# Kernel tuning notes

Hardware: AMD Instinct MI355X
Metric: run time of the kernel (lower is better)

Reference implementation:

```python
import jax, jax.numpy as jnp
import numpy as np


def setup_inputs() -> dict:
    key = jax.random.key(0)
    k1, _ = jax.random.split(key)
    B, H, W, C = 8, 128, 128, 512
    inputs = jax.random.normal(k1, (B, H, W, C), dtype=jnp.float32)
    gamma = jnp.ones((), dtype=jnp.float32)
    return {"inputs": inputs, "gamma": gamma}


def reference(inputs, gamma):
    B, H, W, C = inputs.shape
    q = inputs.reshape(B, H * W, C).astype(jnp.float32)  # [B, HW, C]
    # attention = key @ query = q^T q  -> [B, C, C]
    attn = jnp.einsum('bnc,bnd->bcd', q, q)
    # reversed-softmax trick: softmax(max - attn) over last axis
    attn = jnp.max(attn, axis=-1, keepdims=True) - attn
    attn = jax.nn.softmax(attn, axis=-1)
    # value = query @ attention -> [B, HW, C]
    value = jnp.einsum('bnc,bcd->bnd', q, attn)
    value = value.astype(inputs.dtype).reshape(B, H, W, C)
    return gamma * value + inputs
```

## Files before the change

kernel.cpp:

```cpp
#include <hip/hip_runtime.h>
#include <hip/hip_bf16.h>

#define B_  8
#define C_  512
#define NN  16384
#define SPL 8
#define KB_ (NN / SPL)
#define TT  (KB_ / 64)

typedef _Float16 half8 __attribute__((ext_vector_type(8)));
typedef float    f32x4 __attribute__((ext_vector_type(4)));

__device__ __forceinline__ unsigned short f2h(float x) {
    union { _Float16 h; unsigned short u; } cv;
    cv.h = (_Float16)x;
    return cv.u;
}

__device__ __forceinline__ void gload16(const unsigned short* src, unsigned short* ldst) {
    __builtin_amdgcn_global_load_lds(
        (const __attribute__((address_space(1))) void*)src,
        (__attribute__((address_space(3))) void*)ldst,
        16, 0, 0);
}

__global__ void ws_probe_kernel(float* out, float v) { out[0] = v; }

__global__ __launch_bounds__(256) void pack_kernel(const float* __restrict__ in,
                                                   unsigned short* __restrict__ qT) {
    __shared__ unsigned short lh[64][72];
    int t  = threadIdx.x;
    int n0 = blockIdx.x * 64;
    int c0 = blockIdx.y * 64;
    int b  = blockIdx.z;
    const float* ib = in + ((size_t)b * NN + n0) * C_ + c0;
#pragma unroll
    for (int p = 0; p < 4; ++p) {
        int nl = p * 16 + (t >> 4);
        int cl = (t & 15) * 4;
        float4 v = *(const float4*)(ib + (size_t)nl * C_ + cl);
        lh[cl + 0][nl] = f2h(v.x);
        lh[cl + 1][nl] = f2h(v.y);
        lh[cl + 2][nl] = f2h(v.z);
        lh[cl + 3][nl] = f2h(v.w);
    }
    __syncthreads();
    size_t obase = ((size_t)b * C_ + c0) * NN + n0;
#pragma unroll
    for (int p = 0; p < 2; ++p) {
        int cr = p * 32 + (t >> 3);
        int nf = (t & 7) * 8;
        *(uint4*)(qT + obase + (size_t)cr * NN + nf) = *(const uint4*)&lh[cr][nf];
    }
}

__global__ __launch_bounds__(512, 2) void gram_kernel(const unsigned short* __restrict__ qT,
                                                      float* __restrict__ P) {
    __shared__ unsigned short sA[2][16384];
    __shared__ unsigned short sB[2][16384];
    int t = threadIdx.x, lane = t & 63, wave = t >> 6;
    int wr = wave >> 2, wc = wave & 3;
    int bid = blockIdx.x;
    int b = bid & 7, r = bid >> 3;
    int tile = r & 3, split = r >> 2;
    int tc = tile >> 1, td = tile & 1;
    size_t qb = (size_t)b * C_ * NN;
    const unsigned short* Ap = qT + qb + (size_t)(tc * 256) * NN + (size_t)split * KB_;
    const unsigned short* Bp = qT + qb + (size_t)(td * 256) * NN + (size_t)split * KB_;

    f32x4 acc[8][4];
#pragma unroll
    for (int m = 0; m < 8; ++m)
#pragma unroll
        for (int n = 0; n < 4; ++n) acc[m][n] = (f32x4){0.f, 0.f, 0.f, 0.f};

    int o0 = t * 16,         u0 = o0 ^ (((o0 >> 9) & 1) << 5);
    int o1 = (t + 512) * 16, u1 = o1 ^ (((o1 >> 9) & 1) << 5);
    int rih0 = u0 >> 7, k0 = (u0 & 127) >> 1;
    int rih1 = u1 >> 7, k1 = (u1 & 127) >> 1;

#define STAGE(dst, dd, h, panel, kt)                                                        \
    do {                                                                                    \
        gload16((panel) + (size_t)((h)*128 + rih0) * NN + (kt)*64 + k0,                     \
                &dst[dd][(h)*8192 + t * 8]);                                                \
        gload16((panel) + (size_t)((h)*128 + rih1) * NN + (kt)*64 + k1,                     \
                &dst[dd][(h)*8192 + (t + 512) * 8]);                                        \
    } while (0)

    int g16 = (lane >> 4) * 16;
#define AFRAG(dd, row, ks) \
    (*(const half8*)((const char*)&sA[dd][0] + (((row)*128 + (ks)*64 + g16) ^ (((row)&4) << 3))))
#define BFRAG(dd, row, ks) \
    (*(const half8*)((const char*)&sB[dd][0] + (((row)*128 + (ks)*64 + g16) ^ (((row)&4) << 3))))

    STAGE(sA, 0, 0, Ap, 0);
    STAGE(sB, 0, 0, Bp, 0);
    STAGE(sB, 0, 1, Bp, 0);
    STAGE(sA, 0, 1, Ap, 0);
    asm volatile("s_waitcnt vmcnt(2)" ::: "memory");
    __builtin_amdgcn_s_barrier();

    for (int kt = 0; kt < TT; ++kt) {
        int d = kt & 1, nd = d ^ 1;
        half8 aF[4][2], b0F[2][2], b1F[2][2];
#pragma unroll
        for (int m = 0; m < 4; ++m) {
            int row = wr * 64 + m * 16 + (lane & 15);
#pragma unroll
            for (int ks = 0; ks < 2; ++ks) aF[m][ks] = AFRAG(d, row, ks);
        }
#pragma unroll
        for (int n = 0; n < 2; ++n) {
            int row0 = wc * 32 + n * 16 + (lane & 15);
#pragma unroll
            for (int ks = 0; ks < 2; ++ks) {
                b0F[n][ks] = BFRAG(d, row0, ks);
                b1F[n][ks] = BFRAG(d, (row0 + 128), ks);
            }
        }
        if (kt + 1 < TT) {
            STAGE(sA, nd, 0, Ap, kt + 1);
            STAGE(sB, nd, 0, Bp, kt + 1);
            STAGE(sB, nd, 1, Bp, kt + 1);
        }
        __builtin_amdgcn_s_setprio(1);
#pragma unroll
        for (int m = 0; m < 4; ++m)
#pragma unroll
            for (int n = 0; n < 2; ++n)
#pragma unroll
                for (int ks = 0; ks < 2; ++ks) {
                    acc[m][n]     = __builtin_amdgcn_mfma_f32_16x16x32_f16(aF[m][ks], b0F[n][ks], acc[m][n],     0, 0, 0);
                    acc[m][n + 2] = __builtin_amdgcn_mfma_f32_16x16x32_f16(aF[m][ks], b1F[n][ks], acc[m][n + 2], 0, 0, 0);
                }
        __builtin_amdgcn_s_setprio(0);
        if (kt + 1 < TT) {
            asm volatile("s_waitcnt vmcnt(6)" ::: "memory");
        } else {
            asm volatile("s_waitcnt vmcnt(0)" ::: "memory");
        }
        __builtin_amdgcn_s_barrier();
#pragma unroll
        for (int m = 0; m < 4; ++m) {
            int row = 128 + wr * 64 + m * 16 + (lane & 15);
#pragma unroll
            for (int ks = 0; ks < 2; ++ks) aF[m][ks] = AFRAG(d, row, ks);
        }
        if (kt + 1 < TT) STAGE(sA, nd, 1, Ap, kt + 1);
        __builtin_amdgcn_s_setprio(1);
#pragma unroll
        for (int m = 0; m < 4; ++m)
#pragma unroll
            for (int n = 0; n < 2; ++n)
#pragma unroll
                for (int ks = 0; ks < 2; ++ks) {
                    acc[m + 4][n + 2] = __builtin_amdgcn_mfma_f32_16x16x32_f16(aF[m][ks], b1F[n][ks], acc[m + 4][n + 2], 0, 0, 0);
                    acc[m + 4][n]     = __builtin_amdgcn_mfma_f32_16x16x32_f16(aF[m][ks], b0F[n][ks], acc[m + 4][n],     0, 0, 0);
                }
        __builtin_amdgcn_s_setprio(0);
        asm volatile("s_waitcnt vmcnt(2)" ::: "memory");
        __builtin_amdgcn_s_barrier();
    }

    float* out = P + ((size_t)(split * 8 + b)) * (C_ * C_);
#pragma unroll
    for (int m = 0; m < 8; ++m) {
        int row0 = tc * 256 + wr * 64 + (m & 3) * 16 + (m >> 2) * 128 + (lane >> 4) * 4;
#pragma unroll
        for (int n = 0; n < 4; ++n) {
            int col = td * 256 + wc * 32 + (n & 1) * 16 + (n >> 1) * 128 + (lane & 15);
#pragma unroll
            for (int j = 0; j < 4; ++j)
                out[(size_t)(row0 + j) * C_ + col] = acc[m][n][j];
        }
    }
#undef STAGE
#undef AFRAG
#undef BFRAG
}

__global__ __launch_bounds__(256) void softmax_kernel(const float* __restrict__ P,
                                                      unsigned short* __restrict__ WT) {
    __shared__ unsigned short lw[C_ * 4];
    int t = threadIdx.x, lane = t & 63, wave = t >> 6;
    int b = blockIdx.y;
    int c = blockIdx.x * 4 + wave;
    const float* base = P + (size_t)b * (C_ * C_) + (size_t)c * C_;

    float g[8];
    float mn = 3.4e38f;
#pragma unroll
    for (int k = 0; k < 8; ++k) {
        int d = k * 64 + lane;
        float v = 0.f;
#pragma unroll
        for (int s = 0; s < 8; ++s) v += base[(size_t)s * (8 * C_ * C_) + d];
        g[k] = v;
        mn = fminf(mn, v);
    }
#pragma unroll
    for (int o = 32; o; o >>= 1) mn = fminf(mn, __shfl_xor(mn, o));
    float w[8];
    float sum = 0.f;
#pragma unroll
    for (int k = 0; k < 8; ++k) { w[k] = __expf(mn - g[k]); sum += w[k]; }
#pragma unroll
    for (int o = 32; o; o >>= 1) sum += __shfl_xor(sum, o);
    float inv = 1.0f / sum;
#pragma unroll
    for (int k = 0; k < 8; ++k) {
        int d = k * 64 + lane;
        lw[d * 4 + wave] = f2h(w[k] * inv);
    }
    __syncthreads();
    int c0 = blockIdx.x * 4;
    for (int d = t; d < C_; d += 256)
        *(ushort4*)(WT + ((size_t)b * C_ + d) * C_ + c0) = *(ushort4*)&lw[d * 4];
}

__global__ __launch_bounds__(512, 4) void value_kernel(const float* __restrict__ in,
                                                       const unsigned short* __restrict__ WT,
                                                       const float* __restrict__ gamma,
                                                       float* __restrict__ out) {
    __shared__ unsigned short vA[2][64 * 32];
    __shared__ unsigned short vB[2][512 * 32];
    int t = threadIdx.x, lane = t & 63, wave = t >> 6;
    int wr = wave >> 2, wc = wave & 3;
    int bid = blockIdx.x;
    int b = bid & 7, nt = bid >> 3;
    const float* Ain = in + ((size_t)b * NN + (size_t)nt * 64) * C_;
    const unsigned short* Bin = WT + (size_t)b * C_ * C_;

    f32x4 acc[2][8];
#pragma unroll
    for (int m = 0; m < 2; ++m)
#pragma unroll
        for (int n = 0; n < 8; ++n) acc[m][n] = (f32x4){0.f, 0.f, 0.f, 0.f};

    int boff[4];
#pragma unroll
    for (int p = 0; p < 4; ++p) {
        int o = (t + p * 512) * 16;
        int u = o ^ (((o >> 7) & 3) << 4);
        boff[p] = (u >> 6) * C_ + ((u & 63) >> 1);
    }
    int arow = t >> 2, apart = t & 3;
    bool doA = (t < 256);
    int aoff = arow * C_ + apart * 8;
    int awr  = (arow * 64 + apart * 16) ^ ((arow & 7) << 4);

    auto stageB = [&](int nb, int kt) {
#pragma unroll
        for (int p = 0; p < 4; ++p)
            gload16(Bin + (size_t)boff[p] + kt * 32, &vB[nb][(t + p * 512) * 8]);
    };
    auto loadA = [&](int kt, float4* rg) {
        if (doA) {
            const float* s = Ain + aoff + kt * 32;
            rg[0] = *(const float4*)(s + 0);
            rg[1] = *(const float4*)(s + 4);
        }
    };
    auto writeA = [&](int nb, const float4* rg) {
        if (doA) {
            const float* f = (const float*)rg;
            half8 h;
#pragma unroll
            for (int j = 0; j < 8; ++j) h[j] = (_Float16)f[j];
            *(half8*)((char*)&vA[nb][0] + awr) = h;
        }
    };

    float4 a0[2];
    loadA(0, a0);
    stageB(0, 0);
    writeA(0, a0);
    __syncthreads();

    int g16 = (lane >> 4) * 16;
    for (int kt = 0; kt < 16; ++kt) {
        int cur = kt & 1;
        const char* pa = (const char*)&vA[cur][0];
        const char* pb = (const char*)&vB[cur][0];
        half8 aF[2], bF0[4], bF1[4];
#pragma unroll
        for (int m = 0; m < 2; ++m) {
            int row = wr * 32 + m * 16 + (lane & 15);
            aF[m] = *(const half8*)(pa + ((row * 64 + g16) ^ ((row & 7) << 4)));
        }
#pragma unroll
        for (int n = 0; n < 4; ++n) {
            int row = wc * 128 + n * 16 + (lane & 15);
            bF0[n] = *(const half8*)(pb + ((row * 64 + g16) ^ (((row >> 1) & 3) << 4)));
        }
        float4 an[2];
        if (kt < 15) { loadA(kt + 1, an); stageB(cur ^ 1, kt + 1); }
        __builtin_amdgcn_s_setprio(1);
#pragma unroll
        for (int m = 0; m < 2; ++m)
#pragma unroll
            for (int n = 0; n < 4; ++n)
                acc[m][n] = __builtin_amdgcn_mfma_f32_16x16x32_f16(aF[m], bF0[n], acc[m][n], 0, 0, 0);
        __builtin_amdgcn_s_setprio(0);
#pragma unroll
        for (int n = 0; n < 4; ++n) {
            int row = wc * 128 + (n + 4) * 16 + (lane & 15);
            bF1[n] = *(const half8*)(pb + ((row * 64 + g16) ^ (((row >> 1) & 3) << 4)));
        }
        __builtin_amdgcn_s_setprio(1);
#pragma unroll
        for (int m = 0; m < 2; ++m)
#pragma unroll
            for (int n = 0; n < 4; ++n)
                acc[m][n + 4] = __builtin_amdgcn_mfma_f32_16x16x32_f16(aF[m], bF1[n], acc[m][n + 4], 0, 0, 0);
        __builtin_amdgcn_s_setprio(0);
        if (kt < 15) writeA(cur ^ 1, an);
        __syncthreads();
    }

    float gm = gamma[0];
#pragma unroll
    for (int m = 0; m < 2; ++m) {
        int nrow0 = nt * 64 + wr * 32 + m * 16 + (lane >> 4) * 4;
#pragma unroll
        for (int n = 0; n < 8; ++n) {
            int dd = wc * 128 + n * 16 + (lane & 15);
#pragma unroll
            for (int j = 0; j < 4; ++j) {
                size_t idx = ((size_t)b * NN + (nrow0 + j)) * C_ + dd;
                out[idx] = gm * acc[m][n][j] + in[idx];
            }
        }
    }
}

extern "C" void kernel_launch(void* const* d_in, const int* in_sizes, int n_in,
                              void* d_out, int out_size, void* d_ws, size_t ws_size,
                              hipStream_t stream) {
    const float* in    = (const float*)d_in[0];
    const float* gamma = (const float*)d_in[1];
    float* out = (float*)d_out;

    const size_t q_elems = (size_t)B_ * C_ * NN;
    const size_t need = q_elems * 2
                      + (size_t)SPL * B_ * C_ * C_ * 4
                      + (size_t)B_ * C_ * C_ * 2;
    if (ws_size < need) {
        ws_probe_kernel<<<1, 1, 0, stream>>>(out, (float)ws_size);
        return;
    }

    unsigned short* qT = (unsigned short*)d_ws;
    float* P = (float*)(qT + q_elems);
    unsigned short* WT = (unsigned short*)(P + (size_t)SPL * B_ * C_ * C_);

    pack_kernel<<<dim3(NN / 64, C_ / 64, B_), 256, 0, stream>>>(in, qT);
    gram_kernel<<<256, 512, 0, stream>>>(qT, P);
    softmax_kernel<<<dim3(C_ / 4, B_), 256, 0, stream>>>(P, WT);
    value_kernel<<<2048, 512, 0, stream>>>(in, WT, gamma, out);
}
```

Measured before the change: 350.1 us.

## Stage full fp16 A tile in LDS, read B directly, reuse tile for residual

The value kernel now converts the block's whole 64x512 input tile to fp16 in LDS once, instead of double-buffering 32-wide K slices. B fragments are loaded straight from global memory per lane rather than staged through LDS. This removes the per-iteration barriers from the main loop. The epilogue takes the residual from the fp16 LDS copy instead of re-reading the fp32 input, which saves global traffic but rounds the residual term to fp16. The 64KB of LDS per block may lower occupancy, and the uncoalesced B loads now depend on the cache.

```diff
diff --git a/kernel.cpp b/kernel.cpp
--- a/kernel.cpp
+++ b/kernel.cpp
@@ -222,8 +222,7 @@
                                                        const unsigned short* __restrict__ WT,
                                                        const float* __restrict__ gamma,
                                                        float* __restrict__ out) {
-    __shared__ unsigned short vA[2][64 * 32];
-    __shared__ unsigned short vB[2][512 * 32];
+    __shared__ unsigned short vA[64 * 512];
     int t = threadIdx.x, lane = t & 63, wave = t >> 6;
     int wr = wave >> 2, wc = wave & 3;
     int bid = blockIdx.x;
@@ -231,104 +230,66 @@
     const float* Ain = in + ((size_t)b * NN + (size_t)nt * 64) * C_;
     const unsigned short* Bin = WT + (size_t)b * C_ * C_;
 
+#pragma unroll
+    for (int i = 0; i < 8; ++i) {
+        int chunk = i * 512 + t;
+        int rr = chunk >> 6, c8 = (chunk & 63) * 8;
+        const float* s = Ain + (size_t)rr * C_ + c8;
+        float4 v0 = *(const float4*)s;
+        float4 v1 = *(const float4*)(s + 4);
+        half8 h;
+        h[0] = (_Float16)v0.x; h[1] = (_Float16)v0.y; h[2] = (_Float16)v0.z; h[3] = (_Float16)v0.w;
+        h[4] = (_Float16)v1.x; h[5] = (_Float16)v1.y; h[6] = (_Float16)v1.z; h[7] = (_Float16)v1.w;
+        *(half8*)((char*)vA + ((rr * 1024 + c8 * 2) ^ ((rr & 7) << 4))) = h;
+    }
+    __syncthreads();
+
     f32x4 acc[2][8];
 #pragma unroll
     for (int m = 0; m < 2; ++m)
 #pragma unroll
         for (int n = 0; n < 8; ++n) acc[m][n] = (f32x4){0.f, 0.f, 0.f, 0.f};
 
-    int boff[4];
-#pragma unroll
-    for (int p = 0; p < 4; ++p) {
-        int o = (t + p * 512) * 16;
-        int u = o ^ (((o >> 7) & 3) << 4);
-        boff[p] = (u >> 6) * C_ + ((u & 63) >> 1);
-    }
-    int arow = t >> 2, apart = t & 3;
-    bool doA = (t < 256);
-    int aoff = arow * C_ + apart * 8;
-    int awr  = (arow * 64 + apart * 16) ^ ((arow & 7) << 4);
-
-    auto stageB = [&](int nb, int kt) {
-#pragma unroll
-        for (int p = 0; p < 4; ++p)
-            gload16(Bin + (size_t)boff[p] + kt * 32, &vB[nb][(t + p * 512) * 8]);
-    };
-    auto loadA = [&](int kt, float4* rg) {
-        if (doA) {
-            const float* s = Ain + aoff + kt * 32;
-            rg[0] = *(const float4*)(s + 0);
-            rg[1] = *(const float4*)(s + 4);
-        }
-    };
-    auto writeA = [&](int nb, const float4* rg) {
-        if (doA) {
-            const float* f = (const float*)rg;
-            half8 h;
-#pragma unroll
-            for (int j = 0; j < 8; ++j) h[j] = (_Float16)f[j];
-            *(half8*)((char*)&vA[nb][0] + awr) = h;
-        }
-    };
-
-    float4 a0[2];
-    loadA(0, a0);
-    stageB(0, 0);
-    writeA(0, a0);
-    __syncthreads();
-
     int g16 = (lane >> 4) * 16;
+    int l15 = lane & 15;
+    const unsigned short* Blane = Bin + (size_t)(wc * 128 + l15) * C_ + (lane >> 4) * 8;
+    int ar0 = wr * 32 + l15, ar1 = wr * 32 + 16 + l15;
+
     for (int kt = 0; kt < 16; ++kt) {
-        int cur = kt & 1;
-        const char* pa = (const char*)&vA[cur][0];
-        const char* pb = (const char*)&vB[cur][0];
-        half8 aF[2], bF0[4], bF1[4];
-#pragma unroll
-        for (int m = 0; m < 2; ++m) {
-            int row = wr * 32 + m * 16 + (lane & 15);
-            aF[m] = *(const half8*)(pa + ((row * 64 + g16) ^ ((row & 7) << 4)));
-        }
+        half8 aF0 = *(const half8*)((const char*)vA + ((ar0 * 1024 + kt * 64 + g16) ^ ((ar0 & 7) << 4)));
+        half8 aF1 = *(const half8*)((const char*)vA + ((ar1 * 1024 + kt * 64 + g16) ^ ((ar1 & 7) << 4)));
+        half8 bF[4];
+#pragma unroll
+        for (int n = 0; n < 4; ++n)
+            bF[n] = *(const half8*)(Blane + (size_t)n * 16 * C_ + kt * 32);
 #pragma unroll
         for (int n = 0; n < 4; ++n) {
-            int row = wc * 128 + n * 16 + (lane & 15);
-            bF0[n] = *(const half8*)(pb + ((row * 64 + g16) ^ (((row >> 1) & 3) << 4)));
-        }
-        float4 an[2];
-        if (kt < 15) { loadA(kt + 1, an); stageB(cur ^ 1, kt + 1); }
-        __builtin_amdgcn_s_setprio(1);
-#pragma unroll
-        for (int m = 0; m < 2; ++m)
-#pragma unroll
-            for (int n = 0; n < 4; ++n)
-                acc[m][n] = __builtin_amdgcn_mfma_f32_16x16x32_f16(aF[m], bF0[n], acc[m][n], 0, 0, 0);
-        __builtin_amdgcn_s_setprio(0);
+            acc[0][n] = __builtin_amdgcn_mfma_f32_16x16x32_f16(aF0, bF[n], acc[0][n], 0, 0, 0);
+            acc[1][n] = __builtin_amdgcn_mfma_f32_16x16x32_f16(aF1, bF[n], acc[1][n], 0, 0, 0);
+        }
+#pragma unroll
+        for (int n = 0; n < 4; ++n)
+            bF[n] = *(const half8*)(Blane + (size_t)(n + 4) * 16 * C_ + kt * 32);
 #pragma unroll
         for (int n = 0; n < 4; ++n) {
-            int row = wc * 128 + (n + 4) * 16 + (lane & 15);
-            bF1[n] = *(const half8*)(pb + ((row * 64 + g16) ^ (((row >> 1) & 3) << 4)));
-        }
-        __builtin_amdgcn_s_setprio(1);
-#pragma unroll
-        for (int m = 0; m < 2; ++m)
-#pragma unroll
-            for (int n = 0; n < 4; ++n)
-                acc[m][n + 4] = __builtin_amdgcn_mfma_f32_16x16x32_f16(aF[m], bF1[n], acc[m][n + 4], 0, 0, 0);
-        __builtin_amdgcn_s_setprio(0);
-        if (kt < 15) writeA(cur ^ 1, an);
-        __syncthreads();
+            acc[0][n + 4] = __builtin_amdgcn_mfma_f32_16x16x32_f16(aF0, bF[n], acc[0][n + 4], 0, 0, 0);
+            acc[1][n + 4] = __builtin_amdgcn_mfma_f32_16x16x32_f16(aF1, bF[n], acc[1][n + 4], 0, 0, 0);
+        }
     }
 
     float gm = gamma[0];
 #pragma unroll
     for (int m = 0; m < 2; ++m) {
-        int nrow0 = nt * 64 + wr * 32 + m * 16 + (lane >> 4) * 4;
+        int lr0 = wr * 32 + m * 16 + (lane >> 4) * 4;
 #pragma unroll
         for (int n = 0; n < 8; ++n) {
-            int dd = wc * 128 + n * 16 + (lane & 15);
+            int dd = wc * 128 + n * 16 + l15;
 #pragma unroll
             for (int j = 0; j < 4; ++j) {
-                size_t idx = ((size_t)b * NN + (nrow0 + j)) * C_ + dd;
-                out[idx] = gm * acc[m][n][j] + in[idx];
+                int lr = lr0 + j;
+                float iv = (float)(*(const _Float16*)((const char*)vA +
+                                ((lr * 1024 + dd * 2) ^ ((lr & 7) << 4))));
+                out[((size_t)b * NN + (size_t)nt * 64 + lr) * C_ + dd] = gm * acc[m][n][j] + iv;
             }
         }
     }
```

Measured after the change: 457.8 us. 1.31x slower.
